# Optimization experiments

Hardware: AMD Instinct MI355X
Metric: run time of the kernel (lower is better)

Reference implementation:

```python
import jax, jax.numpy as jnp
import numpy as np

B, D = 256, 131072


def setup_inputs() -> dict:
    key = jax.random.key(0)
    k1, k2 = jax.random.split(key)
    x = jax.random.normal(k1, (B, D), dtype=jnp.float32)
    dropout_noise = jax.random.uniform(k2, (B, D), dtype=jnp.float32)
    return {"x": x, "dropout_noise": dropout_noise}


def reference(x, dropout_noise):
    b = x.shape[0]
    temp = x.reshape(b, -1)
    d = temp.shape[1]

    # torch.corrcoef over rows (rows = variables), values clipped to [-1, 1]
    xm = temp - temp.mean(axis=1, keepdims=True)
    cov = (xm @ xm.T) / (d - 1)                      # [B, B]
    std = jnp.sqrt(jnp.diag(cov))
    corr = jnp.clip(cov / (std[:, None] * std[None, :]), -1.0, 1.0)

    # mean over rows, per-row MSE vs that mean (vectorized loop)
    temp_mean = temp.mean(axis=0)                    # [D]
    row_mse = jnp.mean(jnp.square(temp - temp_mean), axis=1)  # [B]
    total_mse = jnp.sum(row_mse)

    # unique counts of rounded values via sort + adjacent-diff (jit-safe)
    r = jnp.round(temp)
    row_sorted = jnp.sort(r, axis=1)
    row_unique = 1 + jnp.sum(row_sorted[:, 1:] != row_sorted[:, :-1], axis=1)  # [B]
    all_sorted = jnp.sort(r.ravel())
    total_unique = 1 + jnp.sum(all_sorted[1:] != all_sorted[:-1])

    factor1 = jnp.mean(jnp.abs(corr), axis=1)        # [B]
    factor2 = row_mse / total_mse                    # [B]
    factor3 = row_unique.astype(x.dtype) / total_unique.astype(x.dtype)

    candidates = (1.0 - factor1) * factor2 * factor3
    p = jnp.maximum(jnp.max(candidates), 0.0)
    # torch uses p.item(): p is detached from the graph
    p = jax.lax.stop_gradient(p)

    # F.dropout(x, p): keep with prob 1-p, scale by 1/(1-p)
    keep = (dropout_noise >= p).astype(x.dtype)
    return x * keep / (1.0 - p)
```

## Files before the change

kernel.cpp:

```cpp
#include <hip/hip_runtime.h>


#define BR 256
#define DD 131072
#define KBLK 512
#define KS 32
#define NSTG (KBLK / KS)
#define LSTR 40

typedef float f32x4 __attribute__((ext_vector_type(4)));
typedef __bf16 bf16x8 __attribute__((ext_vector_type(8)));
typedef __bf16 bf16x4 __attribute__((ext_vector_type(4)));

__global__ void init_kernel(unsigned long long* __restrict__ pres,
                            double* __restrict__ pscal,
                            float* __restrict__ g32, int zeroG) {
    int t = blockIdx.x * blockDim.x + threadIdx.x;
    if (t < 256) pres[t] = 0ull;
    if (t < 8) pscal[t] = 0.0;
    if (zeroG) {
        for (int j = t; j < 65536; j += gridDim.x * blockDim.x) g32[j] = 0.0f;
    }
}

__device__ __forceinline__ unsigned long long pres_bit(float v) {
    int bi = (int)rintf(v);
    bi = bi < -32 ? -32 : (bi > 31 ? 31 : bi);
    return 1ull << (bi + 32);
}

__device__ __forceinline__ void conv4(float4 v, __bf16* hi, __bf16* lo,
                                      float& rsum, float& lolo,
                                      unsigned long long& mask) {
    float vv[4] = {v.x, v.y, v.z, v.w};
    bf16x4 hv, lv;
#pragma unroll
    for (int k = 0; k < 4; ++k) {
        float f = vv[k];
        __bf16 h = (__bf16)f;
        float hf = (float)h;
        float lof = f - hf;
        __bf16 l = (__bf16)lof;
        float lf = (float)l;
        hv[k] = h;
        lv[k] = l;
        rsum += f;
        lolo += lf * lf;
        mask |= pres_bit(f);
    }
    *(bf16x4*)hi = hv;
    *(bf16x4*)lo = lv;
}

__global__ __launch_bounds__(1024) void gram_kernel(
    const float* __restrict__ x,
    float* __restrict__ gpart,
    float* __restrict__ g32,
    float* __restrict__ rowsumPart,
    float* __restrict__ loloPart,
    unsigned long long* __restrict__ gpres,
    int pathA) {
    __shared__ __bf16 ldsHi[BR * LSTR];
    __shared__ __bf16 ldsLo[BR * LSTR];
    __shared__ float rsbuf[1024];
    __shared__ float lolobuf[1024];
    __shared__ unsigned long long maskbuf[1024];

    const int t = threadIdx.x;
    const int r = t >> 2;
    const int q = t & 3;
    const int lane = t & 63;
    const int wv = t >> 6;
    const int wr = wv >> 2;
    const int wc = wv & 3;
    const int fr = lane & 15;
    const int fq = lane >> 4;
    const int blk = blockIdx.x;

    const float* xrow = x + (size_t)r * DD + (size_t)blk * KBLK;

    f32x4 acc[4][4];
#pragma unroll
    for (int i = 0; i < 4; ++i)
#pragma unroll
        for (int j = 0; j < 4; ++j) acc[i][j] = (f32x4){0.f, 0.f, 0.f, 0.f};

    float rsum = 0.f, lolo = 0.f;
    unsigned long long mask = 0ull;

    const __bf16* aHi = ldsHi + (wr * 64 + fr) * LSTR + fq * 8;
    const __bf16* aLo = ldsLo + (wr * 64 + fr) * LSTR + fq * 8;
    const __bf16* bHi = ldsHi + (wc * 64 + fr) * LSTR + fq * 8;
    const __bf16* bLo = ldsLo + (wc * 64 + fr) * LSTR + fq * 8;

    float4 pre0 = *(const float4*)(xrow + q * 4);
    float4 pre1 = *(const float4*)(xrow + q * 4 + 16);

    for (int s = 0; s < NSTG; ++s) {
        __syncthreads();
        conv4(pre0, &ldsHi[r * LSTR + q * 4], &ldsLo[r * LSTR + q * 4], rsum, lolo, mask);
        conv4(pre1, &ldsHi[r * LSTR + q * 4 + 16], &ldsLo[r * LSTR + q * 4 + 16], rsum, lolo, mask);
        __syncthreads();

        if (s + 1 < NSTG) {
            pre0 = *(const float4*)(xrow + (s + 1) * KS + q * 4);
            pre1 = *(const float4*)(xrow + (s + 1) * KS + q * 4 + 16);
        }

        bf16x8 ah[4], al[4];
#pragma unroll
        for (int i = 0; i < 4; ++i) {
            ah[i] = *(const bf16x8*)(aHi + i * 16 * LSTR);
            al[i] = *(const bf16x8*)(aLo + i * 16 * LSTR);
        }
#pragma unroll
        for (int j = 0; j < 4; ++j) {
            bf16x8 bh = *(const bf16x8*)(bHi + j * 16 * LSTR);
            bf16x8 bl = *(const bf16x8*)(bLo + j * 16 * LSTR);
#pragma unroll
            for (int i = 0; i < 4; ++i) {
                acc[i][j] = __builtin_amdgcn_mfma_f32_16x16x32_bf16(ah[i], bh, acc[i][j], 0, 0, 0);
                acc[i][j] = __builtin_amdgcn_mfma_f32_16x16x32_bf16(ah[i], bl, acc[i][j], 0, 0, 0);
                acc[i][j] = __builtin_amdgcn_mfma_f32_16x16x32_bf16(al[i], bh, acc[i][j], 0, 0, 0);
            }
        }
    }

    __syncthreads();
    rsbuf[t] = rsum;
    lolobuf[t] = lolo;
    maskbuf[t] = mask;
    __syncthreads();
    if (t < 256) {
        float s4 = rsbuf[4 * t] + rsbuf[4 * t + 1] + rsbuf[4 * t + 2] + rsbuf[4 * t + 3];
        float l4 = lolobuf[4 * t] + lolobuf[4 * t + 1] + lolobuf[4 * t + 2] + lolobuf[4 * t + 3];
        unsigned long long m4 = maskbuf[4 * t] | maskbuf[4 * t + 1] |
                                maskbuf[4 * t + 2] | maskbuf[4 * t + 3];
        rowsumPart[blk * 256 + t] = s4;
        loloPart[blk * 256 + t] = l4;
        atomicOr(&gpres[t], m4);
    }

    if (pathA) {
        float* dst = gpart + (size_t)blk * 65536;
#pragma unroll
        for (int i = 0; i < 4; ++i)
#pragma unroll
            for (int j = 0; j < 4; ++j) {
                int row = (wr * 4 + i) * 16 + fq * 4;
                int col = (wc * 4 + j) * 16 + fr;
#pragma unroll
                for (int reg = 0; reg < 4; ++reg)
                    dst[(row + reg) * 256 + col] = acc[i][j][reg];
            }
    } else {
#pragma unroll
        for (int i = 0; i < 4; ++i)
#pragma unroll
            for (int j = 0; j < 4; ++j) {
                int row = (wr * 4 + i) * 16 + fq * 4;
                int col = (wc * 4 + j) * 16 + fr;
#pragma unroll
                for (int reg = 0; reg < 4; ++reg)
                    atomicAdd(&g32[(row + reg) * 256 + col], acc[i][j][reg]);
            }
    }
}

__global__ __launch_bounds__(256) void gred_kernel(const float* __restrict__ gpart,
                                                   double* __restrict__ gf64) {
    int j = blockIdx.x * 256 + threadIdx.x;
    double s = 0.0;
#pragma unroll 8
    for (int p = 0; p < 256; ++p) s += (double)gpart[(size_t)p * 65536 + j];
    gf64[j] = s;
}

__global__ __launch_bounds__(256) void reduce_kernel(
    const double* __restrict__ gf64, const float* __restrict__ g32,
    const float* __restrict__ rsp, const float* __restrict__ lolop,
    const unsigned long long* __restrict__ pres,
    double* __restrict__ pscal, int pathA) {
    __shared__ double rs[256], sd[256], f1s[256], sumg[256], rmse[256], cand[256], gdia[256];
    __shared__ double Ssh, tmse_sh;
    __shared__ int totu_sh;
    const double Dd = (double)DD;
    int i = threadIdx.x;

    double s = 0.0, lol = 0.0;
    for (int p = 0; p < 256; ++p) {
        s += (double)rsp[p * 256 + i];
        lol += (double)lolop[p * 256 + i];
    }
    rs[i] = s;

    double gii = (pathA ? gf64[i * 256 + i] : (double)g32[i * 256 + i]) + lol;
    gdia[i] = gii;
    double covii = (gii - s * s / Dd) / (Dd - 1.0);
    sd[i] = sqrt(covii);
    __syncthreads();

    double f1 = 0.0, sg = 0.0;
    for (int k = 0; k < 256; ++k) {
        double gik = pathA ? gf64[k * 256 + i] : (double)g32[k * 256 + i];
        sg += gik;
        double cov = (gik - rs[i] * rs[k] / Dd) / (Dd - 1.0);
        double corr = cov / (sd[i] * sd[k]);
        corr = fmin(1.0, fmax(-1.0, corr));
        f1 += fabs(corr);
    }
    f1s[i] = f1 / 256.0;
    sumg[i] = sg;
    __syncthreads();

    if (i == 0) {
        double S = 0.0;
        for (int k = 0; k < 256; ++k) S += sumg[k];
        Ssh = S;
        unsigned long long m = 0ull;
        for (int k = 0; k < 256; ++k) m |= pres[k];
        totu_sh = __popcll(m);
    }
    __syncthreads();

    rmse[i] = (gdia[i] - (2.0 / 256.0) * sumg[i] + Ssh / (256.0 * 256.0)) / Dd;
    __syncthreads();
    if (i == 0) {
        double tm = 0.0;
        for (int k = 0; k < 256; ++k) tm += rmse[k];
        tmse_sh = tm;
    }
    __syncthreads();

    double f3 = (double)__popcll(pres[i]) / (double)totu_sh;
    cand[i] = (1.0 - f1s[i]) * (rmse[i] / tmse_sh) * f3;
    __syncthreads();

    if (i == 0) {
        double p = 0.0;
        for (int k = 0; k < 256; ++k) p = fmax(p, cand[k]);
        pscal[0] = p;
        float* pf = (float*)(pscal + 1);
        pf[0] = (float)p;
        pf[1] = (float)(1.0 / (1.0 - p));
    }
}

__global__ __launch_bounds__(256) void dropout_kernel(
    const float4* __restrict__ x, const float4* __restrict__ n,
    float4* __restrict__ o, const double* __restrict__ pscal) {
    const float* pp = (const float*)(pscal + 1);
    const float pf = pp[0];
    const float inv = pp[1];
    int idx = blockIdx.x * 256 + threadIdx.x;
    float4 xv = x[idx];
    float4 nv = n[idx];
    float4 ov;
    ov.x = (nv.x >= pf) ? xv.x * inv : 0.0f;
    ov.y = (nv.y >= pf) ? xv.y * inv : 0.0f;
    ov.z = (nv.z >= pf) ? xv.z * inv : 0.0f;
    ov.w = (nv.w >= pf) ? xv.w * inv : 0.0f;
    o[idx] = ov;
}

extern "C" void kernel_launch(void* const* d_in, const int* in_sizes, int n_in,
                              void* d_out, int out_size, void* d_ws, size_t ws_size,
                              hipStream_t stream) {
    const float* x = (const float*)d_in[0];
    const float* noise = (const float*)d_in[1];
    float* out = (float*)d_out;
    char* ws = (char*)d_ws;

    unsigned long long* pres = (unsigned long long*)(ws + 0);
    double* pscal = (double*)(ws + 2048);
    float* rsp = (float*)(ws + 4096);
    float* lolop = (float*)(ws + 266240);
    float* g32 = (float*)(ws + 528384);
    double* gf64 = (double*)(ws + 790528);
    float* gpart = (float*)(ws + 1314816);

    const size_t needA = 1314816 + (size_t)256 * 65536 * sizeof(float);
    const int pathA = (ws_size >= needA) ? 1 : 0;

    init_kernel<<<64, 256, 0, stream>>>(pres, pscal, g32, !pathA);
    gram_kernel<<<BR, 1024, 0, stream>>>(x, gpart, g32, rsp, lolop, pres, pathA);
    if (pathA) gred_kernel<<<256, 256, 0, stream>>>(gpart, gf64);
    reduce_kernel<<<1, 256, 0, stream>>>(gf64, g32, rsp, lolop, pres, pscal, pathA);
    dropout_kernel<<<(BR * DD) / (4 * 256), 256, 0, stream>>>(
        (const float4*)x, (const float4*)noise, (float4*)out, pscal);
}
```

Baseline: 432.9 us.

## Split single-block reduce into parallel per-row stats, correlation and final kernels

Measured after the change: 359.8 us. 1.2x faster.

```diff
diff --git a/kernel.cpp b/kernel.cpp
--- a/kernel.cpp
+++ b/kernel.cpp
@@ -12,12 +12,41 @@
 typedef __bf16 bf16x8 __attribute__((ext_vector_type(8)));
 typedef __bf16 bf16x4 __attribute__((ext_vector_type(4)));
 
+__device__ __forceinline__ double block_reduce_add_d(double v, double* lds4) {
+    for (int o = 32; o > 0; o >>= 1) v += __shfl_down(v, o, 64);
+    __syncthreads();
+    if ((threadIdx.x & 63) == 0) lds4[threadIdx.x >> 6] = v;
+    __syncthreads();
+    double r = lds4[0] + lds4[1] + lds4[2] + lds4[3];
+    __syncthreads();
+    return r;
+}
+
+__device__ __forceinline__ double block_reduce_max_d(double v, double* lds4) {
+    for (int o = 32; o > 0; o >>= 1) v = fmax(v, __shfl_down(v, o, 64));
+    __syncthreads();
+    if ((threadIdx.x & 63) == 0) lds4[threadIdx.x >> 6] = v;
+    __syncthreads();
+    double r = fmax(fmax(lds4[0], lds4[1]), fmax(lds4[2], lds4[3]));
+    __syncthreads();
+    return r;
+}
+
+__device__ __forceinline__ unsigned long long block_reduce_or_u64(
+    unsigned long long v, unsigned long long* lds4) {
+    for (int o = 32; o > 0; o >>= 1) v |= __shfl_down(v, o, 64);
+    __syncthreads();
+    if ((threadIdx.x & 63) == 0) lds4[threadIdx.x >> 6] = v;
+    __syncthreads();
+    unsigned long long r = lds4[0] | lds4[1] | lds4[2] | lds4[3];
+    __syncthreads();
+    return r;
+}
+
 __global__ void init_kernel(unsigned long long* __restrict__ pres,
-                            double* __restrict__ pscal,
                             float* __restrict__ g32, int zeroG) {
     int t = blockIdx.x * blockDim.x + threadIdx.x;
     if (t < 256) pres[t] = 0ull;
-    if (t < 8) pscal[t] = 0.0;
     if (zeroG) {
         for (int j = t; j < 65536; j += gridDim.x * blockDim.x) g32[j] = 0.0f;
     }
@@ -136,8 +165,8 @@
         float l4 = lolobuf[4 * t] + lolobuf[4 * t + 1] + lolobuf[4 * t + 2] + lolobuf[4 * t + 3];
         unsigned long long m4 = maskbuf[4 * t] | maskbuf[4 * t + 1] |
                                 maskbuf[4 * t + 2] | maskbuf[4 * t + 3];
-        rowsumPart[blk * 256 + t] = s4;
-        loloPart[blk * 256 + t] = l4;
+        rowsumPart[t * 256 + blk] = s4;
+        loloPart[t * 256 + blk] = l4;
         atomicOr(&gpres[t], m4);
     }
 
@@ -167,78 +196,89 @@
     }
 }
 
-__global__ __launch_bounds__(256) void gred_kernel(const float* __restrict__ gpart,
-                                                   double* __restrict__ gf64) {
-    int j = blockIdx.x * 256 + threadIdx.x;
+__global__ __launch_bounds__(256) void gredstats_kernel(
+    const float* __restrict__ gpart, const float* __restrict__ g32,
+    const float* __restrict__ rsp, const float* __restrict__ lolop,
+    double* __restrict__ gf64,
+    double* __restrict__ rsRow, double* __restrict__ sdRow,
+    double* __restrict__ sumgRow, double* __restrict__ giiRow,
+    int pathA) {
+    __shared__ double lds4[4];
+    __shared__ double graw_sh;
+    const int i = blockIdx.x;
+    const int c = threadIdx.x;
+    const double Dd = (double)DD;
+
     double s = 0.0;
+    if (pathA) {
+        const float* src = gpart + (size_t)i * 256 + c;
 #pragma unroll 8
-    for (int p = 0; p < 256; ++p) s += (double)gpart[(size_t)p * 65536 + j];
-    gf64[j] = s;
-}
-
-__global__ __launch_bounds__(256) void reduce_kernel(
-    const double* __restrict__ gf64, const float* __restrict__ g32,
-    const float* __restrict__ rsp, const float* __restrict__ lolop,
+        for (int p = 0; p < 256; ++p) s += (double)src[(size_t)p * 65536];
+    } else {
+        s = (double)g32[i * 256 + c];
+    }
+    gf64[i * 256 + c] = s;
+    if (c == i) graw_sh = s;
+
+    double rs_part = (double)rsp[i * 256 + c];
+    double lolo_part = (double)lolop[i * 256 + c];
+
+    double sumg = block_reduce_add_d(s, lds4);
+    double rs = block_reduce_add_d(rs_part, lds4);
+    double lolo = block_reduce_add_d(lolo_part, lds4);
+
+    if (c == 0) {
+        double gii = graw_sh + lolo;
+        double covii = (gii - rs * rs / Dd) / (Dd - 1.0);
+        rsRow[i] = rs;
+        sdRow[i] = sqrt(covii);
+        sumgRow[i] = sumg;
+        giiRow[i] = gii;
+    }
+}
+
+__global__ __launch_bounds__(256) void f1_kernel(
+    const double* __restrict__ gf64, const double* __restrict__ rsRow,
+    const double* __restrict__ sdRow, double* __restrict__ f1sRow) {
+    __shared__ double lds4[4];
+    const int i = blockIdx.x;
+    const int k = threadIdx.x;
+    const double Dd = (double)DD;
+
+    double gik = gf64[i * 256 + k];
+    double rsi = rsRow[i], rsk = rsRow[k];
+    double sdi = sdRow[i], sdk = sdRow[k];
+    double cov = (gik - rsi * rsk / Dd) / (Dd - 1.0);
+    double corr = cov / (sdi * sdk);
+    corr = fmin(1.0, fmax(-1.0, corr));
+    double f1 = block_reduce_add_d(fabs(corr), lds4);
+    if (k == 0) f1sRow[i] = f1 / 256.0;
+}
+
+__global__ __launch_bounds__(256) void final_kernel(
+    const double* __restrict__ rsRow, const double* __restrict__ sumgRow,
+    const double* __restrict__ giiRow, const double* __restrict__ f1sRow,
     const unsigned long long* __restrict__ pres,
-    double* __restrict__ pscal, int pathA) {
-    __shared__ double rs[256], sd[256], f1s[256], sumg[256], rmse[256], cand[256], gdia[256];
-    __shared__ double Ssh, tmse_sh;
-    __shared__ int totu_sh;
+    double* __restrict__ pscal) {
+    __shared__ double lds4[4];
+    __shared__ unsigned long long lds4u[4];
+    const int t = threadIdx.x;
     const double Dd = (double)DD;
-    int i = threadIdx.x;
-
-    double s = 0.0, lol = 0.0;
-    for (int p = 0; p < 256; ++p) {
-        s += (double)rsp[p * 256 + i];
-        lol += (double)lolop[p * 256 + i];
-    }
-    rs[i] = s;
-
-    double gii = (pathA ? gf64[i * 256 + i] : (double)g32[i * 256 + i]) + lol;
-    gdia[i] = gii;
-    double covii = (gii - s * s / Dd) / (Dd - 1.0);
-    sd[i] = sqrt(covii);
-    __syncthreads();
-
-    double f1 = 0.0, sg = 0.0;
-    for (int k = 0; k < 256; ++k) {
-        double gik = pathA ? gf64[k * 256 + i] : (double)g32[k * 256 + i];
-        sg += gik;
-        double cov = (gik - rs[i] * rs[k] / Dd) / (Dd - 1.0);
-        double corr = cov / (sd[i] * sd[k]);
-        corr = fmin(1.0, fmax(-1.0, corr));
-        f1 += fabs(corr);
-    }
-    f1s[i] = f1 / 256.0;
-    sumg[i] = sg;
-    __syncthreads();
-
-    if (i == 0) {
-        double S = 0.0;
-        for (int k = 0; k < 256; ++k) S += sumg[k];
-        Ssh = S;
-        unsigned long long m = 0ull;
-        for (int k = 0; k < 256; ++k) m |= pres[k];
-        totu_sh = __popcll(m);
-    }
-    __syncthreads();
-
-    rmse[i] = (gdia[i] - (2.0 / 256.0) * sumg[i] + Ssh / (256.0 * 256.0)) / Dd;
-    __syncthreads();
-    if (i == 0) {
-        double tm = 0.0;
-        for (int k = 0; k < 256; ++k) tm += rmse[k];
-        tmse_sh = tm;
-    }
-    __syncthreads();
-
-    double f3 = (double)__popcll(pres[i]) / (double)totu_sh;
-    cand[i] = (1.0 - f1s[i]) * (rmse[i] / tmse_sh) * f3;
-    __syncthreads();
-
-    if (i == 0) {
-        double p = 0.0;
-        for (int k = 0; k < 256; ++k) p = fmax(p, cand[k]);
+
+    double sumg = sumgRow[t];
+    double S = block_reduce_add_d(sumg, lds4);
+    double rmse = (giiRow[t] - (2.0 / 256.0) * sumg + S / (256.0 * 256.0)) / Dd;
+    double tmse = block_reduce_add_d(rmse, lds4);
+
+    unsigned long long m = pres[t];
+    unsigned long long allm = block_reduce_or_u64(m, lds4u);
+    double totu = (double)__popcll(allm);
+    double f3 = (double)__popcll(m) / totu;
+
+    double cand = (1.0 - f1sRow[t]) * (rmse / tmse) * f3;
+    double p = block_reduce_max_d(cand, lds4);
+    if (t == 0) {
+        p = fmax(p, 0.0);
         pscal[0] = p;
         float* pf = (float*)(pscal + 1);
         pf[0] = (float)p;
@@ -273,19 +313,26 @@
 
     unsigned long long* pres = (unsigned long long*)(ws + 0);
     double* pscal = (double*)(ws + 2048);
-    float* rsp = (float*)(ws + 4096);
-    float* lolop = (float*)(ws + 266240);
-    float* g32 = (float*)(ws + 528384);
-    double* gf64 = (double*)(ws + 790528);
-    float* gpart = (float*)(ws + 1314816);
-
-    const size_t needA = 1314816 + (size_t)256 * 65536 * sizeof(float);
+    double* rsRow = (double*)(ws + 4096);
+    double* sdRow = (double*)(ws + 6144);
+    double* sumgRow = (double*)(ws + 8192);
+    double* giiRow = (double*)(ws + 10240);
+    double* f1sRow = (double*)(ws + 12288);
+    float* rsp = (float*)(ws + 16384);
+    float* lolop = (float*)(ws + 278528);
+    double* gf64 = (double*)(ws + 540672);
+    float* gpart = (float*)(ws + 1064960);
+    float* g32 = (float*)(ws + 1064960);
+
+    const size_t needA = 1064960 + (size_t)256 * 65536 * sizeof(float);
     const int pathA = (ws_size >= needA) ? 1 : 0;
 
-    init_kernel<<<64, 256, 0, stream>>>(pres, pscal, g32, !pathA);
+    init_kernel<<<64, 256, 0, stream>>>(pres, g32, !pathA);
     gram_kernel<<<BR, 1024, 0, stream>>>(x, gpart, g32, rsp, lolop, pres, pathA);
-    if (pathA) gred_kernel<<<256, 256, 0, stream>>>(gpart, gf64);
-    reduce_kernel<<<1, 256, 0, stream>>>(gf64, g32, rsp, lolop, pres, pscal, pathA);
+    gredstats_kernel<<<256, 256, 0, stream>>>(gpart, g32, rsp, lolop, gf64,
+                                              rsRow, sdRow, sumgRow, giiRow, pathA);
+    f1_kernel<<<256, 256, 0, stream>>>(gf64, rsRow, sdRow, f1sRow);
+    final_kernel<<<1, 256, 0, stream>>>(rsRow, sumgRow, giiRow, f1sRow, pres, pscal);
     dropout_kernel<<<(BR * DD) / (4 * 256), 256, 0, stream>>>(
         (const float4*)x, (const float4*)noise, (float4*)out, pscal);
 }
```
